# Performance work log

Hardware: AMD Instinct MI355X
Metric: run time of the kernel (lower is better)

## Reference

```python
import jax, jax.numpy as jnp
import numpy as np

OUT_H, OUT_W = 7, 7
SPATIAL_SCALE = 0.25
SAMPLE_NUM = 2
N_ORI = 8
CLOCKWISE = False


def setup_inputs() -> dict:
    key = jax.random.key(0)
    k1, k2, k3, k4, k5 = jax.random.split(key, 5)
    B, Ct, H, W = 2, 256, 256, 256
    n_rois = 512
    features = jax.random.normal(k1, (B, Ct, H, W), dtype=jnp.float32)
    img = H / SPATIAL_SCALE  # image-space extent = 1024
    batch_ind = jax.random.randint(k2, (n_rois,), 0, B).astype(jnp.float32)
    cxy = jax.random.uniform(k3, (n_rois, 2), minval=0.0, maxval=img, dtype=jnp.float32)
    wh = jax.random.uniform(k4, (n_rois, 2), minval=16.0, maxval=img / 4.0, dtype=jnp.float32)
    ang = jax.random.uniform(k5, (n_rois, 1), minval=-np.pi, maxval=np.pi, dtype=jnp.float32)
    rois = jnp.concatenate([batch_ind[:, None], cxy, wh, ang], axis=1)  # (n, 6)
    return {"features": features, "rois": rois}


def _bilinear(feat, y, x):
    # feat: (Ct, H, W); y, x: (P,) -> (Ct, P). Matches mmcv bilinear_interpolate.
    Ct, H, W = feat.shape
    valid = (y >= -1.0) & (y <= H) & (x >= -1.0) & (x <= W)
    y = jnp.maximum(y, 0.0)
    x = jnp.maximum(x, 0.0)
    y0 = jnp.minimum(jnp.floor(y).astype(jnp.int32), H - 1)
    x0 = jnp.minimum(jnp.floor(x).astype(jnp.int32), W - 1)
    y1 = jnp.minimum(y0 + 1, H - 1)
    x1 = jnp.minimum(x0 + 1, W - 1)
    ly = jnp.where(y0 >= H - 1, 0.0, y - y0.astype(y.dtype))
    lx = jnp.where(x0 >= W - 1, 0.0, x - x0.astype(x.dtype))
    hy, hx = 1.0 - ly, 1.0 - lx
    v = ((hy * hx) * feat[:, y0, x0] + (hy * lx) * feat[:, y0, x1]
         + (ly * hx) * feat[:, y1, x0] + (ly * lx) * feat[:, y1, x1])
    return v * valid.astype(feat.dtype)[None, :]


def _per_roi(features, roi):
    B, Ctot, H, W = features.shape
    C = Ctot // N_ORI
    b = roi[0].astype(jnp.int32)
    cx = roi[1] * SPATIAL_SCALE  # roi_center_w
    cy = roi[2] * SPATIAL_SCALE  # roi_center_h
    rw = jnp.maximum(roi[3] * SPATIAL_SCALE, 1.0)
    rh = jnp.maximum(roi[4] * SPATIAL_SCALE, 1.0)
    theta = roi[5]
    bin_h = rh / OUT_H
    bin_w = rw / OUT_W
    # orientation channel alignment (uses un-flipped theta)
    ind_f = theta * N_ORI / (2.0 * jnp.pi)
    ind = jnp.floor(ind_f).astype(jnp.int32)
    l_var = ind_f - ind.astype(theta.dtype)
    r_var = 1.0 - l_var
    ind = jnp.mod(ind, N_ORI)
    th = -theta if CLOCKWISE else theta
    cos_t, sin_t = jnp.cos(th), jnp.sin(th)
    gh = gw = SAMPLE_NUM
    # sample grid in roi-centered coords: yy (OUT_H, gh), xx (OUT_W, gw)
    yy = -rh / 2.0 + (jnp.arange(OUT_H)[:, None] + (jnp.arange(gh) + 0.5) / gh) * bin_h
    xx = -rw / 2.0 + (jnp.arange(OUT_W)[:, None] + (jnp.arange(gw) + 0.5) / gw) * bin_w
    Y = yy[:, None, :, None]  # (OUT_H,1,gh,1)
    X = xx[None, :, None, :]  # (1,OUT_W,1,gw)
    y = (Y * cos_t - X * sin_t + cy).reshape(-1)  # (P,)
    x = (Y * sin_t + X * cos_t + cx).reshape(-1)
    feat = features[b]  # (Ctot, H, W)
    vals = _bilinear(feat, y, x).reshape(C, N_ORI, OUT_H, OUT_W, gh, gw)
    o = jnp.arange(N_ORI)
    idx = jnp.mod(o - ind, N_ORI)
    idx_p = jnp.mod(idx + 1, N_ORI)
    mixed = r_var * vals[:, idx] + l_var * vals[:, idx_p]  # cyclic orientation shift + interp
    out = mixed.mean(axis=(-1, -2))  # average over bin sample grid
    return out.reshape(Ctot, OUT_H, OUT_W)


def reference(features, rois):
    return jax.vmap(lambda r: _per_roi(features, r))(rois)  # (n, Ctot, OUT_H, OUT_W)
```

## Files before the change

### kernel.cpp

```cpp
#include <hip/hip_runtime.h>
#include <hip/hip_fp16.h>
#include <math.h>

#define HH 256
#define WW 256
#define CTOT 256
#define HW (HH * WW)
#define NBIN 49

typedef __attribute__((ext_vector_type(8))) _Float16 half8;

__global__ __launch_bounds__(256) void convert_kernel(
    const float* __restrict__ feats, half8* __restrict__ wsf, int total )
{
    const int g = blockIdx.x * 256 + threadIdx.x;
    if (g >= total) return;
    const int pix = g & (HW - 1);
    const int bc  = g >> 16;
    const float* src = feats + ((size_t)bc * 8) * HW + pix;
    half8 v;
    #pragma unroll
    for (int o = 0; o < 8; ++o) v[o] = (_Float16)src[(size_t)o * HW];
    wsf[g] = v;
}

__global__ __launch_bounds__(256) void riroi_pool_f16(
    const half8* __restrict__ wsf,
    const float* __restrict__ rois,
    float* __restrict__ out,
    int n_rois, int total)
{
    const int g = blockIdx.x * 256 + threadIdx.x;
    if (g >= total) return;
    const int per_cg = n_rois * NBIN;
    const int cg  = g / per_cg;
    const int rem = g - cg * per_cg;
    const int n   = rem / NBIN;
    const int bin = rem - n * NBIN;
    const int ph  = bin / 7;
    const int pw  = bin - ph * 7;

    const float* r = rois + n * 6;
    const int   b     = (int)r[0];
    const float cx    = r[1] * 0.25f;
    const float cy    = r[2] * 0.25f;
    const float rwv   = fmaxf(r[3] * 0.25f, 1.0f);
    const float rhv   = fmaxf(r[4] * 0.25f, 1.0f);
    const float theta = r[5];
    const float bin_h = rhv * (1.0f / 7.0f);
    const float bin_w = rwv * (1.0f / 7.0f);

    const float ind_f = (theta * 8.0f) / 6.28318530717958647692f;
    const int   ind0  = (int)floorf(ind_f);
    const float l_var = ind_f - (float)ind0;
    const float r_var = 1.0f - l_var;
    const int   ind   = ((ind0 % 8) + 8) % 8;
    const float cos_t = cosf(theta);
    const float sin_t = sinf(theta);

    int   off0[4], off1[4];
    float rw0[4], rw1[4], cw0[4], cw1[4];
    #pragma unroll
    for (int s = 0; s < 4; ++s) {
        const int gy = s >> 1, gx = s & 1;
        const float yy = -rhv * 0.5f + ((float)ph + ((float)gy + 0.5f) * 0.5f) * bin_h;
        const float xx = -rwv * 0.5f + ((float)pw + ((float)gx + 0.5f) * 0.5f) * bin_w;
        const float y  = yy * cos_t - xx * sin_t + cy;
        const float x  = yy * sin_t + xx * cos_t + cx;
        const float valid =
            (y >= -1.0f && y <= 256.0f && x >= -1.0f && x <= 256.0f) ? 1.0f : 0.0f;
        const float yc = fmaxf(y, 0.0f);
        const float xc = fmaxf(x, 0.0f);
        const int y0 = min((int)floorf(yc), HH - 1);
        const int x0 = min((int)floorf(xc), WW - 1);
        const int y1 = min(y0 + 1, HH - 1);
        const float ly = (y0 >= HH - 1) ? 0.0f : (yc - (float)y0);
        const float lx = (x0 >= WW - 1) ? 0.0f : (xc - (float)x0);
        const float hy = 1.0f - ly, hx = 1.0f - lx;
        const float sc = 0.25f * valid;
        const int   xb = min(x0, WW - 2);
        cw0[s]  = (x0 < WW - 1) ? hx : 0.0f;
        cw1[s]  = (x0 < WW - 1) ? lx : hx;
        rw0[s]  = hy * sc;
        rw1[s]  = ly * sc;
        off0[s] = (y0 << 8) + xb;
        off1[s] = (y1 << 8) + xb;
    }

    const half8* base = wsf + (size_t)(b * 32 + cg) * HW;

    half8 q[16];
    #pragma unroll
    for (int s = 0; s < 4; ++s) {
        q[s * 4 + 0] = base[off0[s]];
        q[s * 4 + 1] = base[off0[s] + 1];
        q[s * 4 + 2] = base[off1[s]];
        q[s * 4 + 3] = base[off1[s] + 1];
    }

    float acc[8] = {0,0,0,0,0,0,0,0};
    #pragma unroll
    for (int s = 0; s < 4; ++s) {
        const float w00 = rw0[s] * cw0[s];
        const float w01 = rw0[s] * cw1[s];
        const float w10 = rw1[s] * cw0[s];
        const float w11 = rw1[s] * cw1[s];
        const half8 a = q[s * 4 + 0], c = q[s * 4 + 1];
        const half8 d = q[s * 4 + 2], e = q[s * 4 + 3];
        #pragma unroll
        for (int o = 0; o < 8; ++o)
            acc[o] += w00 * (float)a[o] + w01 * (float)c[o]
                    + w10 * (float)d[o] + w11 * (float)e[o];
    }

    float* obase = out + ((size_t)n * CTOT + (size_t)(cg * 8)) * NBIN + bin;
    #pragma unroll
    for (int s = 0; s < 8; ++s) {
        const int o_out = (s + ind) & 7;
        const float val = r_var * acc[s] + l_var * acc[(s + 1) & 7];
        __builtin_nontemporal_store(val, obase + o_out * NBIN);
    }
}

__global__ __launch_bounds__(256) void riroi_rotated_fallback(
    const float* __restrict__ feats, const float* __restrict__ rois,
    float* __restrict__ out, int total)
{
    const int g = blockIdx.x * 256 + threadIdx.x;
    if (g >= total) return;
    const int wpr = 32 * NBIN;
    const int n   = g / wpr;
    const int rem = g - n * wpr;
    const int cg  = rem / NBIN;
    const int bin = rem - cg * NBIN;
    const int ph  = bin / 7;
    const int pw  = bin - ph * 7;
    const float* r = rois + n * 6;
    const int   b     = (int)r[0];
    const float cx    = r[1] * 0.25f;
    const float cy    = r[2] * 0.25f;
    const float rwv   = fmaxf(r[3] * 0.25f, 1.0f);
    const float rhv   = fmaxf(r[4] * 0.25f, 1.0f);
    const float theta = r[5];
    const float bin_h = rhv * (1.0f / 7.0f);
    const float bin_w = rwv * (1.0f / 7.0f);
    const float ind_f = (theta * 8.0f) / 6.28318530717958647692f;
    const int   ind0  = (int)floorf(ind_f);
    const float l_var = ind_f - (float)ind0;
    const float r_var = 1.0f - l_var;
    const int   ind   = ((ind0 % 8) + 8) % 8;
    const float cos_t = cosf(theta);
    const float sin_t = sinf(theta);
    int   off0[4], off1[4];
    float rw0[4], rw1[4], cw0[4], cw1[4];
    #pragma unroll
    for (int s = 0; s < 4; ++s) {
        const int gy = s >> 1, gx = s & 1;
        const float yy = -rhv * 0.5f + ((float)ph + ((float)gy + 0.5f) * 0.5f) * bin_h;
        const float xx = -rwv * 0.5f + ((float)pw + ((float)gx + 0.5f) * 0.5f) * bin_w;
        const float y  = yy * cos_t - xx * sin_t + cy;
        const float x  = yy * sin_t + xx * cos_t + cx;
        const float valid =
            (y >= -1.0f && y <= 256.0f && x >= -1.0f && x <= 256.0f) ? 1.0f : 0.0f;
        const float yc = fmaxf(y, 0.0f);
        const float xc = fmaxf(x, 0.0f);
        const int y0 = min((int)floorf(yc), HH - 1);
        const int x0 = min((int)floorf(xc), WW - 1);
        const int y1 = min(y0 + 1, HH - 1);
        const float ly = (y0 >= HH - 1) ? 0.0f : (yc - (float)y0);
        const float lx = (x0 >= WW - 1) ? 0.0f : (xc - (float)x0);
        const float hy = 1.0f - ly, hx = 1.0f - lx;
        const float sc = 0.25f * valid;
        const int   xb = min(x0, WW - 2);
        cw0[s]  = (x0 < WW - 1) ? hx : 0.0f;
        cw1[s]  = (x0 < WW - 1) ? lx : hx;
        rw0[s]  = hy * sc;
        rw1[s]  = ly * sc;
        off0[s] = (y0 << 8) + xb;
        off1[s] = (y1 << 8) + xb;
    }
    const float* gbase = feats + (size_t)b * (CTOT * HW) + (size_t)(cg * 8) * HW;
    float acc[8];
    #pragma unroll
    for (int o = 0; o < 8; o += 2) {
        const float* pA = gbase + (size_t)o * HW;
        const float* pB = pA + HW;
        float2 q[16];
        #pragma unroll
        for (int s = 0; s < 4; ++s) {
            q[s * 4 + 0] = *(const float2*)(pA + off0[s]);
            q[s * 4 + 1] = *(const float2*)(pA + off1[s]);
            q[s * 4 + 2] = *(const float2*)(pB + off0[s]);
            q[s * 4 + 3] = *(const float2*)(pB + off1[s]);
        }
        float a0 = 0.0f, a1 = 0.0f;
        #pragma unroll
        for (int s = 0; s < 4; ++s) {
            a0 += rw0[s] * (cw0[s] * q[s * 4 + 0].x + cw1[s] * q[s * 4 + 0].y)
                + rw1[s] * (cw0[s] * q[s * 4 + 1].x + cw1[s] * q[s * 4 + 1].y);
            a1 += rw0[s] * (cw0[s] * q[s * 4 + 2].x + cw1[s] * q[s * 4 + 2].y)
                + rw1[s] * (cw0[s] * q[s * 4 + 3].x + cw1[s] * q[s * 4 + 3].y);
        }
        acc[o] = a0; acc[o + 1] = a1;
    }
    float* obase = out + ((size_t)n * CTOT + (size_t)(cg * 8)) * NBIN + bin;
    #pragma unroll
    for (int s = 0; s < 8; ++s) {
        const int o_out = (s + ind) & 7;
        __builtin_nontemporal_store(r_var * acc[s] + l_var * acc[(s + 1) & 7],
                                    obase + o_out * NBIN);
    }
}

extern "C" void kernel_launch(void* const* d_in, const int* in_sizes, int n_in,
                              void* d_out, int out_size, void* d_ws, size_t ws_size,
                              hipStream_t stream) {
    const float* feats = (const float*)d_in[0];
    const float* rois  = (const float*)d_in[1];
    float* out = (float*)d_out;
    const int n_rois = in_sizes[1] / 6;
    const int B      = in_sizes[0] / (CTOT * HW);
    const int total  = n_rois * 32 * NBIN;
    const size_t ws_need = (size_t)B * 32 * HW * sizeof(half8);

    if (ws_size >= ws_need) {
        half8* wsf = (half8*)d_ws;
        const int tc = B * 32 * HW;
        convert_kernel<<<(tc + 255) / 256, 256, 0, stream>>>(feats, wsf, tc);
        riroi_pool_f16<<<(total + 255) / 256, 256, 0, stream>>>(wsf, rois, out, n_rois, total);
    } else {
        riroi_rotated_fallback<<<(total + 255) / 256, 256, 0, stream>>>(feats, rois, out, total);
    }
}
```

Before: 256.4 us.

## Vectorize fp16 conversion and split bin samples across four lanes with shuffle reduction

```diff
diff --git a/kernel.cpp b/kernel.cpp
--- a/kernel.cpp
+++ b/kernel.cpp
@@ -9,34 +9,45 @@
 #define NBIN 49
 
 typedef __attribute__((ext_vector_type(8))) _Float16 half8;
-
-__global__ __launch_bounds__(256) void convert_kernel(
-    const float* __restrict__ feats, half8* __restrict__ wsf, int total )
+typedef __attribute__((ext_vector_type(4))) float fvec4;
+
+__global__ __launch_bounds__(256) void convert_kernel_v2(
+    const float* __restrict__ feats, half8* __restrict__ wsf, int total4 )
 {
     const int g = blockIdx.x * 256 + threadIdx.x;
-    if (g >= total) return;
-    const int pix = g & (HW - 1);
-    const int bc  = g >> 16;
+    if (g >= total4) return;
+    const int pix = (g & 16383) << 2;
+    const int bc  = g >> 14;
     const float* src = feats + ((size_t)bc * 8) * HW + pix;
-    half8 v;
-    #pragma unroll
-    for (int o = 0; o < 8; ++o) v[o] = (_Float16)src[(size_t)o * HW];
-    wsf[g] = v;
-}
-
-__global__ __launch_bounds__(256) void riroi_pool_f16(
+    fvec4 v[8];
+    #pragma unroll
+    for (int o = 0; o < 8; ++o)
+        v[o] = __builtin_nontemporal_load((const fvec4*)(src + (size_t)o * HW));
+    half8* dst = wsf + (size_t)bc * HW + pix;
+    #pragma unroll
+    for (int j = 0; j < 4; ++j) {
+        half8 h;
+        h[0] = (_Float16)v[0][j]; h[1] = (_Float16)v[1][j];
+        h[2] = (_Float16)v[2][j]; h[3] = (_Float16)v[3][j];
+        h[4] = (_Float16)v[4][j]; h[5] = (_Float16)v[5][j];
+        h[6] = (_Float16)v[6][j]; h[7] = (_Float16)v[7][j];
+        dst[j] = h;
+    }
+}
+
+__global__ __launch_bounds__(256) void riroi_pool_f16_v3(
     const half8* __restrict__ wsf,
     const float* __restrict__ rois,
     float* __restrict__ out,
-    int n_rois, int total)
+    int per_cg4)
 {
-    const int g = blockIdx.x * 256 + threadIdx.x;
-    if (g >= total) return;
-    const int per_cg = n_rois * NBIN;
-    const int cg  = g / per_cg;
-    const int rem = g - cg * per_cg;
-    const int n   = rem / NBIN;
-    const int bin = rem - n * NBIN;
+    const int h = blockIdx.x * 256 + threadIdx.x;
+    if (h >= per_cg4) return;
+    const int cg  = blockIdx.y;
+    const int s   = h & 3;
+    const int t   = h >> 2;
+    const int n   = t / NBIN;
+    const int bin = t - n * NBIN;
     const int ph  = bin / 7;
     const int pw  = bin - ph * 7;
 
@@ -58,67 +69,69 @@
     const float cos_t = cosf(theta);
     const float sin_t = sinf(theta);
 
-    int   off0[4], off1[4];
-    float rw0[4], rw1[4], cw0[4], cw1[4];
-    #pragma unroll
-    for (int s = 0; s < 4; ++s) {
-        const int gy = s >> 1, gx = s & 1;
-        const float yy = -rhv * 0.5f + ((float)ph + ((float)gy + 0.5f) * 0.5f) * bin_h;
-        const float xx = -rwv * 0.5f + ((float)pw + ((float)gx + 0.5f) * 0.5f) * bin_w;
-        const float y  = yy * cos_t - xx * sin_t + cy;
-        const float x  = yy * sin_t + xx * cos_t + cx;
-        const float valid =
-            (y >= -1.0f && y <= 256.0f && x >= -1.0f && x <= 256.0f) ? 1.0f : 0.0f;
-        const float yc = fmaxf(y, 0.0f);
-        const float xc = fmaxf(x, 0.0f);
-        const int y0 = min((int)floorf(yc), HH - 1);
-        const int x0 = min((int)floorf(xc), WW - 1);
-        const int y1 = min(y0 + 1, HH - 1);
-        const float ly = (y0 >= HH - 1) ? 0.0f : (yc - (float)y0);
-        const float lx = (x0 >= WW - 1) ? 0.0f : (xc - (float)x0);
-        const float hy = 1.0f - ly, hx = 1.0f - lx;
-        const float sc = 0.25f * valid;
-        const int   xb = min(x0, WW - 2);
-        cw0[s]  = (x0 < WW - 1) ? hx : 0.0f;
-        cw1[s]  = (x0 < WW - 1) ? lx : hx;
-        rw0[s]  = hy * sc;
-        rw1[s]  = ly * sc;
-        off0[s] = (y0 << 8) + xb;
-        off1[s] = (y1 << 8) + xb;
-    }
+    const int gy = s >> 1, gx = s & 1;
+    const float yy = -rhv * 0.5f + ((float)ph + ((float)gy + 0.5f) * 0.5f) * bin_h;
+    const float xx = -rwv * 0.5f + ((float)pw + ((float)gx + 0.5f) * 0.5f) * bin_w;
+    const float y  = yy * cos_t - xx * sin_t + cy;
+    const float x  = yy * sin_t + xx * cos_t + cx;
+    const float valid =
+        (y >= -1.0f && y <= 256.0f && x >= -1.0f && x <= 256.0f) ? 1.0f : 0.0f;
+    const float yc = fmaxf(y, 0.0f);
+    const float xc = fmaxf(x, 0.0f);
+    const int y0 = min((int)floorf(yc), HH - 1);
+    const int x0 = min((int)floorf(xc), WW - 1);
+    const int y1 = min(y0 + 1, HH - 1);
+    const float ly = (y0 >= HH - 1) ? 0.0f : (yc - (float)y0);
+    const float lx = (x0 >= WW - 1) ? 0.0f : (xc - (float)x0);
+    const float hy = 1.0f - ly, hx = 1.0f - lx;
+    const float sc = 0.25f * valid;
+    const int   xb = min(x0, WW - 2);
+    const float cw0 = (x0 < WW - 1) ? hx : 0.0f;
+    const float cw1 = (x0 < WW - 1) ? lx : hx;
+    const float w00 = hy * sc * cw0;
+    const float w01 = hy * sc * cw1;
+    const float w10 = ly * sc * cw0;
+    const float w11 = ly * sc * cw1;
+    const int off0 = (y0 << 8) + xb;
+    const int off1 = (y1 << 8) + xb;
 
     const half8* base = wsf + (size_t)(b * 32 + cg) * HW;
 
-    half8 q[16];
-    #pragma unroll
-    for (int s = 0; s < 4; ++s) {
-        q[s * 4 + 0] = base[off0[s]];
-        q[s * 4 + 1] = base[off0[s] + 1];
-        q[s * 4 + 2] = base[off1[s]];
-        q[s * 4 + 3] = base[off1[s] + 1];
-    }
-
-    float acc[8] = {0,0,0,0,0,0,0,0};
-    #pragma unroll
-    for (int s = 0; s < 4; ++s) {
-        const float w00 = rw0[s] * cw0[s];
-        const float w01 = rw0[s] * cw1[s];
-        const float w10 = rw1[s] * cw0[s];
-        const float w11 = rw1[s] * cw1[s];
-        const half8 a = q[s * 4 + 0], c = q[s * 4 + 1];
-        const half8 d = q[s * 4 + 2], e = q[s * 4 + 3];
-        #pragma unroll
-        for (int o = 0; o < 8; ++o)
-            acc[o] += w00 * (float)a[o] + w01 * (float)c[o]
-                    + w10 * (float)d[o] + w11 * (float)e[o];
+    const half8 q0 = base[off0];
+    const half8 q1 = base[off0 + 1];
+    const half8 q2 = base[off1];
+    const half8 q3 = base[off1 + 1];
+
+    float acc[8];
+    #pragma unroll
+    for (int o = 0; o < 8; ++o)
+        acc[o] = w00 * (float)q0[o] + w01 * (float)q1[o]
+               + w10 * (float)q2[o] + w11 * (float)q3[o];
+
+    #pragma unroll
+    for (int o = 0; o < 8; ++o) {
+        acc[o] += __shfl_xor(acc[o], 1, 64);
+        acc[o] += __shfl_xor(acc[o], 2, 64);
     }
 
     float* obase = out + ((size_t)n * CTOT + (size_t)(cg * 8)) * NBIN + bin;
-    #pragma unroll
-    for (int s = 0; s < 8; ++s) {
-        const int o_out = (s + ind) & 7;
-        const float val = r_var * acc[s] + l_var * acc[(s + 1) & 7];
-        __builtin_nontemporal_store(val, obase + o_out * NBIN);
+    switch (s) {
+    case 0:
+        __builtin_nontemporal_store(r_var * acc[0] + l_var * acc[1], obase + (((0 + ind) & 7) * NBIN));
+        __builtin_nontemporal_store(r_var * acc[1] + l_var * acc[2], obase + (((1 + ind) & 7) * NBIN));
+        break;
+    case 1:
+        __builtin_nontemporal_store(r_var * acc[2] + l_var * acc[3], obase + (((2 + ind) & 7) * NBIN));
+        __builtin_nontemporal_store(r_var * acc[3] + l_var * acc[4], obase + (((3 + ind) & 7) * NBIN));
+        break;
+    case 2:
+        __builtin_nontemporal_store(r_var * acc[4] + l_var * acc[5], obase + (((4 + ind) & 7) * NBIN));
+        __builtin_nontemporal_store(r_var * acc[5] + l_var * acc[6], obase + (((5 + ind) & 7) * NBIN));
+        break;
+    default:
+        __builtin_nontemporal_store(r_var * acc[6] + l_var * acc[7], obase + (((6 + ind) & 7) * NBIN));
+        __builtin_nontemporal_store(r_var * acc[7] + l_var * acc[0], obase + (((7 + ind) & 7) * NBIN));
+        break;
     }
 }
 
@@ -220,15 +233,17 @@
     float* out = (float*)d_out;
     const int n_rois = in_sizes[1] / 6;
     const int B      = in_sizes[0] / (CTOT * HW);
-    const int total  = n_rois * 32 * NBIN;
     const size_t ws_need = (size_t)B * 32 * HW * sizeof(half8);
 
     if (ws_size >= ws_need) {
         half8* wsf = (half8*)d_ws;
-        const int tc = B * 32 * HW;
-        convert_kernel<<<(tc + 255) / 256, 256, 0, stream>>>(feats, wsf, tc);
-        riroi_pool_f16<<<(total + 255) / 256, 256, 0, stream>>>(wsf, rois, out, n_rois, total);
+        const int tc4 = B * 32 * HW / 4;
+        convert_kernel_v2<<<(tc4 + 255) / 256, 256, 0, stream>>>(feats, wsf, tc4);
+        const int per_cg4 = n_rois * NBIN * 4;
+        dim3 grid((per_cg4 + 255) / 256, 32);
+        riroi_pool_f16_v3<<<grid, 256, 0, stream>>>(wsf, rois, out, per_cg4);
     } else {
+        const int total = n_rois * 32 * NBIN;
         riroi_rotated_fallback<<<(total + 255) / 256, 256, 0, stream>>>(feats, rois, out, total);
     }
 }
```

Result: faster. 239.0 us (-6.8%).
